# Kernel optimization log

Measured on AMD Instinct MI355X. Metric: run time of the kernel, lower is better.

The kernel has to match this reference:

```python
import jax, jax.numpy as jnp
import numpy as np

B, S, E = 2, 2048, 1024
H = 16
HD = E // H  # head_dim = 64


def setup_inputs() -> dict:
    key = jax.random.key(0)
    ks = jax.random.split(key, 10)
    x = jax.random.normal(ks[0], (B, S, E), dtype=jnp.float32)
    # key-padding mask: True means position is masked out
    mask = jax.random.randint(ks[1], (B, 1, 1, S), 0, 2).astype(jnp.bool_)
    scale = 0.02
    Wq = jax.random.normal(ks[2], (E, E), dtype=jnp.float32) * scale
    bq = jnp.zeros((E,), dtype=jnp.float32)
    Wk = jax.random.normal(ks[3], (E, E), dtype=jnp.float32) * scale
    bk = jnp.zeros((E,), dtype=jnp.float32)
    Wv = jax.random.normal(ks[4], (E, E), dtype=jnp.float32) * scale
    bv = jnp.zeros((E,), dtype=jnp.float32)
    Wo = jax.random.normal(ks[5], (E, E), dtype=jnp.float32) * scale
    bo = jnp.zeros((E,), dtype=jnp.float32)
    return {"x": x, "mask": mask, "Wq": Wq, "bq": bq, "Wk": Wk, "bk": bk,
            "Wv": Wv, "bv": bv, "Wo": Wo, "bo": bo}


def reference(x, mask, Wq, bq, Wk, bk, Wv, bv, Wo, bo):
    b, s, e = x.shape
    # QKV projections (torch Linear: y = x @ W.T + b), split into heads
    q = (x @ Wq.T + bq).reshape(b, s, H, HD).transpose(0, 2, 1, 3)  # [B,H,S,D]
    k = (x @ Wk.T + bk).reshape(b, s, H, HD).transpose(0, 2, 1, 3)
    v = (x @ Wv.T + bv).reshape(b, s, H, HD).transpose(0, 2, 1, 3)
    scores = jnp.einsum('bhqd,bhkd->bhqk', q, k) / jnp.sqrt(jnp.float32(HD))
    scores = jnp.where(mask, jnp.float32(-1e9), scores)
    probs = jax.nn.softmax(scores, axis=-1)
    attn = jnp.einsum('bhqk,bhkd->bhqd', probs, v)  # [B,H,S,D]
    attn = attn.transpose(0, 2, 1, 3).reshape(b, s, e)  # merge heads -> [B,S,E]
    out = attn @ Wo.T + bo  # dropout p=0 (eval) -> identity
    return out
```

## Files before the change

### kernel.cpp

```cpp
#include <hip/hip_runtime.h>
#include <hip/hip_bf16.h>
#include <math.h>

#define BATCH 2
#define SEQ   2048
#define EMB   1024
#define NH    16
#define HD    64
#define K_DIM 1024
#define QSCALE 0.18033688011f

typedef __hip_bfloat16 bf16;
typedef __attribute__((ext_vector_type(8))) short short8;
typedef __attribute__((ext_vector_type(4))) short short4v;
typedef __attribute__((ext_vector_type(4))) float f32x4;

__device__ inline short f2bf(float f){ bf16 h=__float2bfloat16(f); return *(short*)&h; }

__global__ __launch_bounds__(256)
void cvt_pack(const float* __restrict__ x,  const float* __restrict__ wq,
              const float* __restrict__ wk, const float* __restrict__ wv,
              const float* __restrict__ wo, short* __restrict__ dst)
{
    size_t gid = ((size_t)blockIdx.x * 256 + threadIdx.x) * 4;
    int seg = (int)(gid >> 20);
    const float* src; size_t off;
    if (seg < 4)       { src = x;  off = gid; }
    else if (seg == 4) { src = wq; off = gid - ((size_t)4 << 20); }
    else if (seg == 5) { src = wk; off = gid - ((size_t)5 << 20); }
    else if (seg == 6) { src = wv; off = gid - ((size_t)6 << 20); }
    else               { src = wo; off = gid - ((size_t)7 << 20); }
    f32x4 v = *(const f32x4*)(src + off);
    short4v s;
    for (int j = 0; j < 4; ++j) s[j] = f2bf(v[j]);
    *(short4v*)(dst + gid) = s;
}

__global__ __launch_bounds__(256)
void gemm_qkv_fused(const bf16* __restrict__ xb, const bf16* __restrict__ wb,
                    const float* __restrict__ bq, const float* __restrict__ bk_,
                    const float* __restrict__ bv_, bf16* __restrict__ q,
                    bf16* __restrict__ kt, bf16* __restrict__ vt)
{
    __shared__ __align__(16) short As[128 * 40];
    __shared__ __align__(16) short Bs[128 * 40];

    const int tid  = threadIdx.x;
    const int proj = blockIdx.x >> 3;
    const int n0   = (blockIdx.x & 7) * 128;
    const int m0   = blockIdx.y * 128;
    const bf16* W  = wb + ((size_t)proj << 20);
    const float* bias = (proj == 0) ? bq : (proj == 1) ? bk_ : bv_;

    const int wave = tid >> 6, lane = tid & 63;
    const int wm = wave >> 1, wn = wave & 1;
    const int lr = lane & 15, lg = lane >> 4;
    const int r0 = tid >> 2, c8 = (tid & 3) * 8;

    f32x4 acc[4][4];
    for (int mi = 0; mi < 4; ++mi)
        for (int ni = 0; ni < 4; ++ni) acc[mi][ni] = (f32x4){0.f,0.f,0.f,0.f};

    short8 pa[2], pb[2];
    auto ld = [&](int k0) {
        pa[0] = *(const short8*)&xb[(size_t)(m0 + r0)      * K_DIM + k0 + c8];
        pa[1] = *(const short8*)&xb[(size_t)(m0 + r0 + 64) * K_DIM + k0 + c8];
        pb[0] = *(const short8*)&W [(size_t)(n0 + r0)      * K_DIM + k0 + c8];
        pb[1] = *(const short8*)&W [(size_t)(n0 + r0 + 64) * K_DIM + k0 + c8];
    };
    ld(0);

    for (int k0 = 0; k0 < K_DIM; k0 += 32) {
        *(short8*)&As[r0 * 40 + c8]        = pa[0];
        *(short8*)&As[(r0 + 64) * 40 + c8] = pa[1];
        *(short8*)&Bs[r0 * 40 + c8]        = pb[0];
        *(short8*)&Bs[(r0 + 64) * 40 + c8] = pb[1];
        __syncthreads();
        if (k0 + 32 < K_DIM) ld(k0 + 32);

        short8 af[4], bf_[4];
        for (int mi = 0; mi < 4; ++mi)
            af[mi]  = *(const short8*)&As[(wm * 64 + mi * 16 + lr) * 40 + lg * 8];
        for (int ni = 0; ni < 4; ++ni)
            bf_[ni] = *(const short8*)&Bs[(wn * 64 + ni * 16 + lr) * 40 + lg * 8];
        for (int mi = 0; mi < 4; ++mi)
            for (int ni = 0; ni < 4; ++ni)
                acc[mi][ni] = __builtin_amdgcn_mfma_f32_16x16x32_bf16(
                    af[mi], bf_[ni], acc[mi][ni], 0, 0, 0);
        __syncthreads();
    }

    for (int mi = 0; mi < 4; ++mi)
        for (int ni = 0; ni < 4; ++ni) {
            int n = n0 + wn * 64 + ni * 16 + lr;
            float bvv = bias[n];
            int h = n >> 6, d = n & 63;
            int mbase = m0 + wm * 64 + mi * 16 + lg * 4;
            int b = mbase >> 11;
            if (proj == 0) {
                for (int r = 0; r < 4; ++r) {
                    int s = (mbase + r) & 2047;
                    q[((((size_t)b * NH) + h) * SEQ + s) * HD + d] =
                        __float2bfloat16((acc[mi][ni][r] + bvv) * QSCALE);
                }
            } else if (proj == 1) {
                for (int r = 0; r < 4; ++r) {
                    int s = (mbase + r) & 2047;
                    kt[((((size_t)b * NH) + h) * SEQ + s) * HD + d] =
                        __float2bfloat16(acc[mi][ni][r] + bvv);
                }
            } else {
                int s = mbase & 2047;
                short4v pk;
                for (int r = 0; r < 4; ++r) pk[r] = f2bf(acc[mi][ni][r] + bvv);
                *(short4v*)((short*)vt + ((((size_t)b * NH) + h) * HD + d) * SEQ + s) = pk;
            }
        }
}

__global__ __launch_bounds__(256)
void gemm_out64(const bf16* __restrict__ A, const bf16* __restrict__ W,
                const float* __restrict__ bias, float* __restrict__ C)
{
    __shared__ __align__(16) short As[128 * 40];
    __shared__ __align__(16) short Bs[64 * 40];

    const int tid = threadIdx.x;
    const int n0  = blockIdx.x * 64;
    const int m0  = blockIdx.y * 128;
    const int wave = tid >> 6, lane = tid & 63;
    const int wm = wave >> 1, wn = wave & 1;
    const int lr = lane & 15, lg = lane >> 4;
    const int r0 = tid >> 2, c8 = (tid & 3) * 8;

    f32x4 acc[4][2];
    for (int mi = 0; mi < 4; ++mi)
        for (int ni = 0; ni < 2; ++ni) acc[mi][ni] = (f32x4){0.f,0.f,0.f,0.f};

    short8 pa[2], pb;
    auto ld = [&](int k0) {
        pa[0] = *(const short8*)&A[(size_t)(m0 + r0)      * K_DIM + k0 + c8];
        pa[1] = *(const short8*)&A[(size_t)(m0 + r0 + 64) * K_DIM + k0 + c8];
        pb    = *(const short8*)&W[(size_t)(n0 + r0)      * K_DIM + k0 + c8];
    };
    ld(0);

    for (int k0 = 0; k0 < K_DIM; k0 += 32) {
        *(short8*)&As[r0 * 40 + c8]        = pa[0];
        *(short8*)&As[(r0 + 64) * 40 + c8] = pa[1];
        *(short8*)&Bs[r0 * 40 + c8]        = pb;
        __syncthreads();
        if (k0 + 32 < K_DIM) ld(k0 + 32);

        short8 af[4], bf_[2];
        for (int mi = 0; mi < 4; ++mi)
            af[mi]  = *(const short8*)&As[(wm * 64 + mi * 16 + lr) * 40 + lg * 8];
        for (int ni = 0; ni < 2; ++ni)
            bf_[ni] = *(const short8*)&Bs[(wn * 32 + ni * 16 + lr) * 40 + lg * 8];
        for (int mi = 0; mi < 4; ++mi)
            for (int ni = 0; ni < 2; ++ni)
                acc[mi][ni] = __builtin_amdgcn_mfma_f32_16x16x32_bf16(
                    af[mi], bf_[ni], acc[mi][ni], 0, 0, 0);
        __syncthreads();
    }

    for (int mi = 0; mi < 4; ++mi)
        for (int ni = 0; ni < 2; ++ni) {
            int n = n0 + wn * 32 + ni * 16 + lr;
            float bvv = bias[n];
            int mbase = m0 + wm * 64 + mi * 16 + lg * 4;
            for (int r = 0; r < 4; ++r)
                C[(size_t)(mbase + r) * EMB + n] = acc[mi][ni][r] + bvv;
        }
}

__global__ __launch_bounds__(256)
void attn_flash2(const bf16* __restrict__ q, const bf16* __restrict__ k,
                 const bf16* __restrict__ vt, const int* __restrict__ mask,
                 bf16* __restrict__ attn)
{
    __shared__ __align__(16) bf16 Qs[128][HD + 8];
    __shared__ __align__(16) bf16 Ks[64][HD + 8];
    __shared__ __align__(16) bf16 Vt[HD][64 + 8];
    __shared__ __align__(16) bf16 Ps[128][64 + 8];
    __shared__ int maskI[64];

    const int q0   = blockIdx.x * 128;
    const int h    = blockIdx.y;
    const int b    = blockIdx.z;
    const int tid  = threadIdx.x;
    const int lane = tid & 63;
    const int wave = tid >> 6;
    const int wq0  = wave * 32;
    const int lr   = lane & 15;
    const int lg   = lane >> 4;

    const size_t bh  = ((size_t)b * NH + h) * SEQ;
    const size_t bhd = ((size_t)b * NH + h) * HD;

    for (int i = 0; i < 4; ++i) {
        int e = tid + i * 256;
        int r = e >> 3, c = (e & 7) * 8;
        *(short8*)&Qs[r][c] = *(const short8*)&q[(bh + q0 + r) * HD + c];
    }
    __syncthreads();

    short8 aq[2][2];
    for (int mi = 0; mi < 2; ++mi) {
        aq[mi][0] = *(const short8*)&Qs[wq0 + mi * 16 + lr][lg * 8];
        aq[mi][1] = *(const short8*)&Qs[wq0 + mi * 16 + lr][32 + lg * 8];
    }

    short8 ones;
    for (int j = 0; j < 8; ++j) ones[j] = (short)0x3F80;

    f32x4 o[2][4], lacc[2];
    for (int mi = 0; mi < 2; ++mi) {
        lacc[mi] = (f32x4){0.f,0.f,0.f,0.f};
        for (int db = 0; db < 4; ++db) o[mi][db] = (f32x4){0.f,0.f,0.f,0.f};
    }

    short8 pk[2], pv[2];
    int pm = 0;
    auto ld = [&](int k0) {
        for (int i = 0; i < 2; ++i) {
            int e = tid + i * 256;
            int r = e >> 3, c = (e & 7) * 8;
            pk[i] = *(const short8*)&k [(bh + k0 + r) * HD + c];
            pv[i] = *(const short8*)&vt[(bhd + r) * SEQ + k0 + c];
        }
        if (tid < 64) pm = mask[(size_t)b * SEQ + k0 + tid];
    };
    ld(0);

    for (int k0 = 0; k0 < SEQ; k0 += 64) {
        for (int i = 0; i < 2; ++i) {
            int e = tid + i * 256;
            int r = e >> 3, c = (e & 7) * 8;
            *(short8*)&Ks[r][c] = pk[i];
            *(short8*)&Vt[r][c] = pv[i];
        }
        if (tid < 64) maskI[tid] = pm;
        __syncthreads();
        if (k0 + 64 < SEQ) ld(k0 + 64);

        f32x4 c_[2][4];
        for (int cb = 0; cb < 4; ++cb) {
            short8 b0 = *(const short8*)&Ks[cb * 16 + lr][lg * 8];
            short8 b1 = *(const short8*)&Ks[cb * 16 + lr][32 + lg * 8];
            for (int mi = 0; mi < 2; ++mi) {
                f32x4 cc = (f32x4){0.f,0.f,0.f,0.f};
                cc = __builtin_amdgcn_mfma_f32_16x16x32_bf16(aq[mi][0], b0, cc, 0, 0, 0);
                cc = __builtin_amdgcn_mfma_f32_16x16x32_bf16(aq[mi][1], b1, cc, 0, 0, 0);
                c_[mi][cb] = cc;
            }
        }

        float mb[4];
        for (int cb = 0; cb < 4; ++cb)
            mb[cb] = maskI[cb * 16 + lr] ? -1e30f : 0.f;
        for (int mi = 0; mi < 2; ++mi)
            for (int cb = 0; cb < 4; ++cb)
                for (int r = 0; r < 4; ++r) {
                    float p = exp2f(c_[mi][cb][r] + mb[cb]);
                    Ps[wq0 + mi * 16 + lg * 4 + r][cb * 16 + lr] = __float2bfloat16(p);
                }

        short8 ap[2][2];
        for (int mi = 0; mi < 2; ++mi) {
            ap[mi][0] = *(const short8*)&Ps[wq0 + mi * 16 + lr][lg * 8];
            ap[mi][1] = *(const short8*)&Ps[wq0 + mi * 16 + lr][32 + lg * 8];
        }
        for (int db = 0; db < 4; ++db) {
            short8 bv0 = *(const short8*)&Vt[db * 16 + lr][lg * 8];
            short8 bv1 = *(const short8*)&Vt[db * 16 + lr][32 + lg * 8];
            for (int mi = 0; mi < 2; ++mi) {
                o[mi][db] = __builtin_amdgcn_mfma_f32_16x16x32_bf16(ap[mi][0], bv0, o[mi][db], 0, 0, 0);
                o[mi][db] = __builtin_amdgcn_mfma_f32_16x16x32_bf16(ap[mi][1], bv1, o[mi][db], 0, 0, 0);
            }
        }
        for (int mi = 0; mi < 2; ++mi) {
            lacc[mi] = __builtin_amdgcn_mfma_f32_16x16x32_bf16(ap[mi][0], ones, lacc[mi], 0, 0, 0);
            lacc[mi] = __builtin_amdgcn_mfma_f32_16x16x32_bf16(ap[mi][1], ones, lacc[mi], 0, 0, 0);
        }
        __syncthreads();
    }

    for (int mi = 0; mi < 2; ++mi) {
        f32x4 linv;
        for (int r = 0; r < 4; ++r) linv[r] = 1.f / lacc[mi][r];
        for (int db = 0; db < 4; ++db)
            for (int r = 0; r < 4; ++r) {
                int srow = q0 + wq0 + mi * 16 + lg * 4 + r;
                int col  = h * HD + db * 16 + lr;
                attn[((size_t)b * SEQ + srow) * EMB + col] =
                    __float2bfloat16(o[mi][db][r] * linv[r]);
            }
    }
}

extern "C" void kernel_launch(void* const* d_in, const int* in_sizes, int n_in,
                              void* d_out, int out_size, void* d_ws, size_t ws_size,
                              hipStream_t stream)
{
    const float* x    = (const float*)d_in[0];
    const int*   mask = (const int*)d_in[1];
    const float* Wq   = (const float*)d_in[2];
    const float* bq   = (const float*)d_in[3];
    const float* Wk   = (const float*)d_in[4];
    const float* bk   = (const float*)d_in[5];
    const float* Wv   = (const float*)d_in[6];
    const float* bv   = (const float*)d_in[7];
    const float* Wo   = (const float*)d_in[8];
    const float* bo   = (const float*)d_in[9];
    float* out = (float*)d_out;

    const size_t TENS = (size_t)BATCH * SEQ * EMB;
    bf16* q    = (bf16*)d_ws;
    bf16* kt   = q    + TENS;
    bf16* vt   = kt   + TENS;
    bf16* attn = vt   + TENS;
    bf16* xb   = attn + TENS;
    bf16* wb   = xb   + TENS;

    cvt_pack<<<8192, 256, 0, stream>>>(x, Wq, Wk, Wv, Wo, (short*)xb);

    gemm_qkv_fused<<<dim3(24, 32), 256, 0, stream>>>(xb, wb, bq, bk, bv, q, kt, vt);

    attn_flash2<<<dim3(SEQ / 128, NH, BATCH), 256, 0, stream>>>(q, kt, vt, mask, attn);

    gemm_out64<<<dim3(16, 32), 256, 0, stream>>>(attn, wb + ((size_t)3 << 20), bo, out);
}
```

Measured before the change: 224.5 us.

## Use direct global-to-LDS loads in GEMMs and transpose score layout in attention

Both GEMM kernels now issue buffer-to-LDS direct loads (global_load_lds, 16 bytes per lane) into unpadded 32-wide tiles instead of staging through registers with a padded layout. This drops the register prefetch, so loads are no longer overlapped with the MFMA of the previous tile, and the unpadded rows may cause LDS bank conflicts. The attention kernel swaps the MFMA operand order so scores come out transposed, which lets each lane write P as packed 4-wide stores. It also reuses the Q shared buffer for P and precomputes the mask as a float bias to cut LDS footprint.

```diff
diff --git a/kernel.cpp b/kernel.cpp
--- a/kernel.cpp
+++ b/kernel.cpp
@@ -16,6 +16,12 @@
 typedef __attribute__((ext_vector_type(4))) float f32x4;
 
 __device__ inline short f2bf(float f){ bf16 h=__float2bfloat16(f); return *(short*)&h; }
+
+__device__ __forceinline__ void gld_lds16(const bf16* g, bf16* l) {
+    __builtin_amdgcn_global_load_lds(
+        (const __attribute__((address_space(1))) unsigned int*)g,
+        (__attribute__((address_space(3))) unsigned int*)l, 16, 0, 0);
+}
 
 __global__ __launch_bounds__(256)
 void cvt_pack(const float* __restrict__ x,  const float* __restrict__ wq,
@@ -37,13 +43,13 @@
 }
 
 __global__ __launch_bounds__(256)
-void gemm_qkv_fused(const bf16* __restrict__ xb, const bf16* __restrict__ wb,
-                    const float* __restrict__ bq, const float* __restrict__ bk_,
-                    const float* __restrict__ bv_, bf16* __restrict__ q,
-                    bf16* __restrict__ kt, bf16* __restrict__ vt)
-{
-    __shared__ __align__(16) short As[128 * 40];
-    __shared__ __align__(16) short Bs[128 * 40];
+void gemm_qkv2(const bf16* __restrict__ xb, const bf16* __restrict__ wb,
+               const float* __restrict__ bq, const float* __restrict__ bk_,
+               const float* __restrict__ bv_, bf16* __restrict__ q,
+               bf16* __restrict__ kt, bf16* __restrict__ vt)
+{
+    __shared__ __align__(16) bf16 As[128 * 32];
+    __shared__ __align__(16) bf16 Bs[128 * 32];
 
     const int tid  = threadIdx.x;
     const int proj = blockIdx.x >> 3;
@@ -55,34 +61,25 @@
     const int wave = tid >> 6, lane = tid & 63;
     const int wm = wave >> 1, wn = wave & 1;
     const int lr = lane & 15, lg = lane >> 4;
-    const int r0 = tid >> 2, c8 = (tid & 3) * 8;
+    const int srow = lane >> 2;
+    const int scol = (lane & 3) * 8;
 
     f32x4 acc[4][4];
     for (int mi = 0; mi < 4; ++mi)
         for (int ni = 0; ni < 4; ++ni) acc[mi][ni] = (f32x4){0.f,0.f,0.f,0.f};
 
-    short8 pa[2], pb[2];
-    auto ld = [&](int k0) {
-        pa[0] = *(const short8*)&xb[(size_t)(m0 + r0)      * K_DIM + k0 + c8];
-        pa[1] = *(const short8*)&xb[(size_t)(m0 + r0 + 64) * K_DIM + k0 + c8];
-        pb[0] = *(const short8*)&W [(size_t)(n0 + r0)      * K_DIM + k0 + c8];
-        pb[1] = *(const short8*)&W [(size_t)(n0 + r0 + 64) * K_DIM + k0 + c8];
-    };
-    ld(0);
-
     for (int k0 = 0; k0 < K_DIM; k0 += 32) {
-        *(short8*)&As[r0 * 40 + c8]        = pa[0];
-        *(short8*)&As[(r0 + 64) * 40 + c8] = pa[1];
-        *(short8*)&Bs[r0 * 40 + c8]        = pb[0];
-        *(short8*)&Bs[(r0 + 64) * 40 + c8] = pb[1];
-        __syncthreads();
-        if (k0 + 32 < K_DIM) ld(k0 + 32);
-
+        for (int i = 0; i < 2; ++i) {
+            int rb = (wave * 2 + i) * 16;
+            gld_lds16(&xb[(size_t)(m0 + rb + srow) * K_DIM + k0 + scol], &As[rb * 32]);
+            gld_lds16(&W [(size_t)(n0 + rb + srow) * K_DIM + k0 + scol], &Bs[rb * 32]);
+        }
+        __syncthreads();
         short8 af[4], bf_[4];
         for (int mi = 0; mi < 4; ++mi)
-            af[mi]  = *(const short8*)&As[(wm * 64 + mi * 16 + lr) * 40 + lg * 8];
+            af[mi]  = *(const short8*)&As[(wm * 64 + mi * 16 + lr) * 32 + lg * 8];
         for (int ni = 0; ni < 4; ++ni)
-            bf_[ni] = *(const short8*)&Bs[(wn * 64 + ni * 16 + lr) * 40 + lg * 8];
+            bf_[ni] = *(const short8*)&Bs[(wn * 64 + ni * 16 + lr) * 32 + lg * 8];
         for (int mi = 0; mi < 4; ++mi)
             for (int ni = 0; ni < 4; ++ni)
                 acc[mi][ni] = __builtin_amdgcn_mfma_f32_16x16x32_bf16(
@@ -119,11 +116,11 @@
 }
 
 __global__ __launch_bounds__(256)
-void gemm_out64(const bf16* __restrict__ A, const bf16* __restrict__ W,
-                const float* __restrict__ bias, float* __restrict__ C)
-{
-    __shared__ __align__(16) short As[128 * 40];
-    __shared__ __align__(16) short Bs[64 * 40];
+void gemm_out2(const bf16* __restrict__ A, const bf16* __restrict__ W,
+               const float* __restrict__ bias, float* __restrict__ C)
+{
+    __shared__ __align__(16) bf16 As[128 * 32];
+    __shared__ __align__(16) bf16 Bs[64 * 32];
 
     const int tid = threadIdx.x;
     const int n0  = blockIdx.x * 64;
@@ -131,32 +128,27 @@
     const int wave = tid >> 6, lane = tid & 63;
     const int wm = wave >> 1, wn = wave & 1;
     const int lr = lane & 15, lg = lane >> 4;
-    const int r0 = tid >> 2, c8 = (tid & 3) * 8;
+    const int srow = lane >> 2, scol = (lane & 3) * 8;
 
     f32x4 acc[4][2];
     for (int mi = 0; mi < 4; ++mi)
         for (int ni = 0; ni < 2; ++ni) acc[mi][ni] = (f32x4){0.f,0.f,0.f,0.f};
 
-    short8 pa[2], pb;
-    auto ld = [&](int k0) {
-        pa[0] = *(const short8*)&A[(size_t)(m0 + r0)      * K_DIM + k0 + c8];
-        pa[1] = *(const short8*)&A[(size_t)(m0 + r0 + 64) * K_DIM + k0 + c8];
-        pb    = *(const short8*)&W[(size_t)(n0 + r0)      * K_DIM + k0 + c8];
-    };
-    ld(0);
-
     for (int k0 = 0; k0 < K_DIM; k0 += 32) {
-        *(short8*)&As[r0 * 40 + c8]        = pa[0];
-        *(short8*)&As[(r0 + 64) * 40 + c8] = pa[1];
-        *(short8*)&Bs[r0 * 40 + c8]        = pb;
-        __syncthreads();
-        if (k0 + 32 < K_DIM) ld(k0 + 32);
-
+        for (int i = 0; i < 2; ++i) {
+            int rb = (wave * 2 + i) * 16;
+            gld_lds16(&A[(size_t)(m0 + rb + srow) * K_DIM + k0 + scol], &As[rb * 32]);
+        }
+        {
+            int rb = wave * 16;
+            gld_lds16(&W[(size_t)(n0 + rb + srow) * K_DIM + k0 + scol], &Bs[rb * 32]);
+        }
+        __syncthreads();
         short8 af[4], bf_[2];
         for (int mi = 0; mi < 4; ++mi)
-            af[mi]  = *(const short8*)&As[(wm * 64 + mi * 16 + lr) * 40 + lg * 8];
+            af[mi]  = *(const short8*)&As[(wm * 64 + mi * 16 + lr) * 32 + lg * 8];
         for (int ni = 0; ni < 2; ++ni)
-            bf_[ni] = *(const short8*)&Bs[(wn * 32 + ni * 16 + lr) * 40 + lg * 8];
+            bf_[ni] = *(const short8*)&Bs[(wn * 32 + ni * 16 + lr) * 32 + lg * 8];
         for (int mi = 0; mi < 4; ++mi)
             for (int ni = 0; ni < 2; ++ni)
                 acc[mi][ni] = __builtin_amdgcn_mfma_f32_16x16x32_bf16(
@@ -175,15 +167,14 @@
 }
 
 __global__ __launch_bounds__(256)
-void attn_flash2(const bf16* __restrict__ q, const bf16* __restrict__ k,
+void attn_flash3(const bf16* __restrict__ q, const bf16* __restrict__ k,
                  const bf16* __restrict__ vt, const int* __restrict__ mask,
                  bf16* __restrict__ attn)
 {
-    __shared__ __align__(16) bf16 Qs[128][HD + 8];
-    __shared__ __align__(16) bf16 Ks[64][HD + 8];
-    __shared__ __align__(16) bf16 Vt[HD][64 + 8];
-    __shared__ __align__(16) bf16 Ps[128][64 + 8];
-    __shared__ int maskI[64];
+    __shared__ __align__(16) bf16 QP[128][72];
+    __shared__ __align__(16) bf16 Ks[64][72];
+    __shared__ __align__(16) bf16 Vt[64][72];
+    __shared__ float maskF[64];
 
     const int q0   = blockIdx.x * 128;
     const int h    = blockIdx.y;
@@ -201,14 +192,14 @@
     for (int i = 0; i < 4; ++i) {
         int e = tid + i * 256;
         int r = e >> 3, c = (e & 7) * 8;
-        *(short8*)&Qs[r][c] = *(const short8*)&q[(bh + q0 + r) * HD + c];
+        *(short8*)&QP[r][c] = *(const short8*)&q[(bh + q0 + r) * HD + c];
     }
     __syncthreads();
 
-    short8 aq[2][2];
+    short8 bq_[2][2];
     for (int mi = 0; mi < 2; ++mi) {
-        aq[mi][0] = *(const short8*)&Qs[wq0 + mi * 16 + lr][lg * 8];
-        aq[mi][1] = *(const short8*)&Qs[wq0 + mi * 16 + lr][32 + lg * 8];
+        bq_[mi][0] = *(const short8*)&QP[wq0 + mi * 16 + lr][lg * 8];
+        bq_[mi][1] = *(const short8*)&QP[wq0 + mi * 16 + lr][32 + lg * 8];
     }
 
     short8 ones;
@@ -220,14 +211,14 @@
         for (int db = 0; db < 4; ++db) o[mi][db] = (f32x4){0.f,0.f,0.f,0.f};
     }
 
-    short8 pk[2], pv[2];
+    short8 pk_[2], pv_[2];
     int pm = 0;
     auto ld = [&](int k0) {
         for (int i = 0; i < 2; ++i) {
             int e = tid + i * 256;
             int r = e >> 3, c = (e & 7) * 8;
-            pk[i] = *(const short8*)&k [(bh + k0 + r) * HD + c];
-            pv[i] = *(const short8*)&vt[(bhd + r) * SEQ + k0 + c];
+            pk_[i] = *(const short8*)&k [(bh + k0 + r) * HD + c];
+            pv_[i] = *(const short8*)&vt[(bhd + r) * SEQ + k0 + c];
         }
         if (tid < 64) pm = mask[(size_t)b * SEQ + k0 + tid];
     };
@@ -237,39 +228,39 @@
         for (int i = 0; i < 2; ++i) {
             int e = tid + i * 256;
             int r = e >> 3, c = (e & 7) * 8;
-            *(short8*)&Ks[r][c] = pk[i];
-            *(short8*)&Vt[r][c] = pv[i];
-        }
-        if (tid < 64) maskI[tid] = pm;
+            *(short8*)&Ks[r][c] = pk_[i];
+            *(short8*)&Vt[r][c] = pv_[i];
+        }
+        if (tid < 64) maskF[tid] = pm ? -1e30f : 0.f;
         __syncthreads();
         if (k0 + 64 < SEQ) ld(k0 + 64);
 
-        f32x4 c_[2][4];
+        f32x4 st[2][4];
         for (int cb = 0; cb < 4; ++cb) {
-            short8 b0 = *(const short8*)&Ks[cb * 16 + lr][lg * 8];
-            short8 b1 = *(const short8*)&Ks[cb * 16 + lr][32 + lg * 8];
+            short8 a0 = *(const short8*)&Ks[cb * 16 + lr][lg * 8];
+            short8 a1 = *(const short8*)&Ks[cb * 16 + lr][32 + lg * 8];
             for (int mi = 0; mi < 2; ++mi) {
                 f32x4 cc = (f32x4){0.f,0.f,0.f,0.f};
-                cc = __builtin_amdgcn_mfma_f32_16x16x32_bf16(aq[mi][0], b0, cc, 0, 0, 0);
-                cc = __builtin_amdgcn_mfma_f32_16x16x32_bf16(aq[mi][1], b1, cc, 0, 0, 0);
-                c_[mi][cb] = cc;
-            }
-        }
-
-        float mb[4];
-        for (int cb = 0; cb < 4; ++cb)
-            mb[cb] = maskI[cb * 16 + lr] ? -1e30f : 0.f;
-        for (int mi = 0; mi < 2; ++mi)
-            for (int cb = 0; cb < 4; ++cb)
-                for (int r = 0; r < 4; ++r) {
-                    float p = exp2f(c_[mi][cb][r] + mb[cb]);
-                    Ps[wq0 + mi * 16 + lg * 4 + r][cb * 16 + lr] = __float2bfloat16(p);
-                }
+                cc = __builtin_amdgcn_mfma_f32_16x16x32_bf16(a0, bq_[mi][0], cc, 0, 0, 0);
+                cc = __builtin_amdgcn_mfma_f32_16x16x32_bf16(a1, bq_[mi][1], cc, 0, 0, 0);
+                st[mi][cb] = cc;
+            }
+        }
+
+        for (int cb = 0; cb < 4; ++cb) {
+            f32x4 mb = *(const f32x4*)&maskF[cb * 16 + lg * 4];
+            for (int mi = 0; mi < 2; ++mi) {
+                short4v pkv;
+                for (int r = 0; r < 4; ++r)
+                    pkv[r] = f2bf(exp2f(st[mi][cb][r] + mb[r]));
+                *(short4v*)&QP[wq0 + mi * 16 + lr][cb * 16 + lg * 4] = pkv;
+            }
+        }
 
         short8 ap[2][2];
         for (int mi = 0; mi < 2; ++mi) {
-            ap[mi][0] = *(const short8*)&Ps[wq0 + mi * 16 + lr][lg * 8];
-            ap[mi][1] = *(const short8*)&Ps[wq0 + mi * 16 + lr][32 + lg * 8];
+            ap[mi][0] = *(const short8*)&QP[wq0 + mi * 16 + lr][lg * 8];
+            ap[mi][1] = *(const short8*)&QP[wq0 + mi * 16 + lr][32 + lg * 8];
         }
         for (int db = 0; db < 4; ++db) {
             short8 bv0 = *(const short8*)&Vt[db * 16 + lr][lg * 8];
@@ -325,9 +316,9 @@
 
     cvt_pack<<<8192, 256, 0, stream>>>(x, Wq, Wk, Wv, Wo, (short*)xb);
 
-    gemm_qkv_fused<<<dim3(24, 32), 256, 0, stream>>>(xb, wb, bq, bk, bv, q, kt, vt);
-
-    attn_flash2<<<dim3(SEQ / 128, NH, BATCH), 256, 0, stream>>>(q, kt, vt, mask, attn);
-
-    gemm_out64<<<dim3(16, 32), 256, 0, stream>>>(attn, wb + ((size_t)3 << 20), bo, out);
-}
+    gemm_qkv2<<<dim3(24, 32), 256, 0, stream>>>(xb, wb, bq, bk, bv, q, kt, vt);
+
+    attn_flash3<<<dim3(SEQ / 128, NH, BATCH), 256, 0, stream>>>(q, kt, vt, mask, attn);
+
+    gemm_out2<<<dim3(16, 32), 256, 0, stream>>>(attn, wb + ((size_t)3 << 20), bo, out);
+}
```

New measurement: 214.9 us. 4.3% less time.
